# Optimization experiments

Hardware: AMD Instinct MI355X
Metric: run time of the kernel (lower is better)

Reference implementation:

```python
import jax, jax.numpy as jnp
import numpy as np

B, S, D = 2, 4096, 512
H, DK, DV = 8, 64, 64
LN_EPS = 1e-5
ATTN_EPS = 1e-6


def layer_norm(x, g, b):
    mu = jnp.mean(x, axis=-1, keepdims=True)
    var = jnp.var(x, axis=-1, keepdims=True)
    return (x - mu) * jax.lax.rsqrt(var + LN_EPS) * g + b


def setup_inputs() -> dict:
    key = jax.random.key(0)
    ks = jax.random.split(key, 12)
    s = 1.0 / np.sqrt(D)
    inp = {
        "Q": jax.random.normal(ks[0], (B, S, D), jnp.float32),
        "K": jax.random.normal(ks[1], (B, S, D), jnp.float32),
        "V": jax.random.normal(ks[2], (B, S, D), jnp.float32),
        "W_q": jax.random.normal(ks[3], (D, H * DK), jnp.float32) * s,
        "W_k": jax.random.normal(ks[4], (D, H * DK), jnp.float32) * s,
        "W_v": jax.random.normal(ks[5], (D, H * DV), jnp.float32) * s,
        "W_o": jax.random.normal(ks[6], (H * DV, D), jnp.float32) * s,
        "ln1_g": jnp.ones((D,), jnp.float32),
        "ln1_b": jnp.zeros((D,), jnp.float32),
        "ln2_g": jnp.ones((D,), jnp.float32),
        "ln2_b": jnp.zeros((D,), jnp.float32),
        "w1": jax.random.normal(ks[7], (4 * D, D), jnp.float32) * s,  # torch Linear: (out, in)
        "b1": jnp.zeros((4 * D,), jnp.float32),
        "w2": jax.random.normal(ks[8], (D, 4 * D), jnp.float32) * (1.0 / np.sqrt(4 * D)),
        "b2": jnp.zeros((D,), jnp.float32),
    }
    return inp


def reference(Q, K, V, W_q, W_k, W_v, W_o, ln1_g, ln1_b, ln2_g, ln2_b, w1, b1, w2, b2):
    Qn = layer_norm(Q, ln1_g, ln1_b)
    # project and split heads: [B,S,H,dk] -> [B,H,S,dk]
    q = (Qn @ W_q).reshape(B, S, H, DK).transpose(0, 2, 1, 3)
    k = (K @ W_k).reshape(B, S, H, DK).transpose(0, 2, 1, 3)
    v = (V @ W_v).reshape(B, S, H, DV).transpose(0, 2, 1, 3)
    scores = jnp.einsum("bhqd,bhkd->bhqk", q, k) / (np.sqrt(DK) + ATTN_EPS)
    attn = jax.nn.softmax(scores, axis=-1)  # same as max-subtract softmax
    ctx = jnp.einsum("bhqk,bhkd->bhqd", attn, v)
    ctx = ctx.transpose(0, 2, 1, 3).reshape(B, S, H * DV)
    att_out = ctx @ W_o  # dropout = identity (eval)
    X = Q + att_out
    Xn = layer_norm(X, ln2_g, ln2_b)
    h = jax.nn.gelu(Xn @ w1.T + b1, approximate=False)
    ffn = h @ w2.T + b2
    return X + ffn
```

## Files before the change

kernel.cpp:

```cpp
#include <hip/hip_runtime.h>

typedef unsigned short u16;
typedef __attribute__((ext_vector_type(8))) short short8;
typedef __attribute__((ext_vector_type(4))) float f32x4;

struct __align__(8) us4 { u16 x, y, z, w; };
struct __align__(8) ui2 { unsigned x, y; };

#define CEXP (1.44269504089f / (8.0f + 1e-6f))

__device__ __forceinline__ u16 f2bf(float f) {
  unsigned u = __builtin_bit_cast(unsigned, f);
  unsigned r = (u + 0x7FFFu + ((u >> 16) & 1u)) >> 16;
  return (u16)r;
}

__device__ __forceinline__ unsigned pack_bf2_trunc(float a, float b) {
  return __builtin_amdgcn_perm(__builtin_bit_cast(unsigned, b),
                               __builtin_bit_cast(unsigned, a), 0x07060302u);
}

__device__ __forceinline__ void async_load16(const void* g, void* l) {
  __builtin_amdgcn_global_load_lds((const __attribute__((address_space(1))) void*)g,
                                   (__attribute__((address_space(3))) void*)l, 16, 0, 0);
}

__global__ void prep_weights(const float* __restrict__ Wq, const float* __restrict__ Wk,
                             const float* __restrict__ Wv, const float* __restrict__ Wo,
                             const float* __restrict__ w1, const float* __restrict__ w2,
                             u16* __restrict__ wqkvT, u16* __restrict__ woT,
                             u16* __restrict__ w1b, u16* __restrict__ w2b) {
  const int z = blockIdx.y;
  const int stride = gridDim.x * blockDim.x;
  const int i0 = blockIdx.x * blockDim.x + threadIdx.x;
  if (z < 4) {
    const float* src = z == 0 ? Wq : z == 1 ? Wk : z == 2 ? Wv : Wo;
    u16* dst = z < 3 ? wqkvT + z * 512 * 512 : woT;
    const float scale = (z == 0) ? CEXP : 1.0f;
    for (int i = i0; i < 512 * 512; i += stride) {
      int k = i >> 9, n = i & 511;
      dst[(size_t)n * 512 + k] = f2bf(src[i] * scale);
    }
  } else {
    const float* src = z == 4 ? w1 : w2;
    u16* dst = z == 4 ? w1b : w2b;
    for (int i = i0; i < 2048 * 512; i += stride) dst[i] = f2bf(src[i]);
  }
}

template <bool KV>
__launch_bounds__(128)
__global__ void ln_cast(const float* __restrict__ X, const float* __restrict__ gw,
                        const float* __restrict__ bw, u16* __restrict__ Y,
                        const float* __restrict__ Kin, const float* __restrict__ Vin,
                        u16* __restrict__ Kb, u16* __restrict__ Vb) {
  const int row = blockIdx.x, t = threadIdx.x;
  const size_t base = (size_t)row * 512;
  float4 x = ((const float4*)(X + base))[t];
  float s = x.x + x.y + x.z + x.w;
  float ss = x.x * x.x + x.y * x.y + x.z * x.z + x.w * x.w;
#pragma unroll
  for (int off = 32; off > 0; off >>= 1) {
    s += __shfl_xor(s, off);
    ss += __shfl_xor(ss, off);
  }
  __shared__ float red[4];
  if ((t & 63) == 0) { red[(t >> 6) * 2] = s; red[(t >> 6) * 2 + 1] = ss; }
  __syncthreads();
  const float tot = red[0] + red[2], tss = red[1] + red[3];
  const float mu = tot * (1.0f / 512.0f);
  const float var = tss * (1.0f / 512.0f) - mu * mu;
  const float rs = rsqrtf(var + 1e-5f);
  float4 g4 = ((const float4*)gw)[t];
  float4 b4 = ((const float4*)bw)[t];
  us4 o;
  o.x = f2bf((x.x - mu) * rs * g4.x + b4.x);
  o.y = f2bf((x.y - mu) * rs * g4.y + b4.y);
  o.z = f2bf((x.z - mu) * rs * g4.z + b4.z);
  o.w = f2bf((x.w - mu) * rs * g4.w + b4.w);
  ((us4*)(Y + base))[t] = o;
  if constexpr (KV) {
    float4 k4 = ((const float4*)(Kin + base))[t];
    float4 v4 = ((const float4*)(Vin + base))[t];
    us4 ko, vo;
    ko.x = f2bf(k4.x); ko.y = f2bf(k4.y); ko.z = f2bf(k4.z); ko.w = f2bf(k4.w);
    vo.x = f2bf(v4.x); vo.y = f2bf(v4.y); vo.z = f2bf(v4.z); vo.w = f2bf(v4.w);
    ((us4*)(Kb + base))[t] = ko;
    ((us4*)(Vb + base))[t] = vo;
  }
}

__launch_bounds__(256, 3)
__global__ void gemm_qkv(const u16* __restrict__ Aq, const u16* __restrict__ Ak,
                         const u16* __restrict__ Av, const u16* __restrict__ Bt,
                         u16* __restrict__ qb, u16* __restrict__ kb, u16* __restrict__ vtb) {
  __shared__ __align__(16) u16 sA[128 * 32];
  __shared__ __align__(16) u16 sB[128 * 32];
  const int tid = threadIdx.x;
  const int wave = tid >> 6, lane = tid & 63;
  const int l15 = lane & 15, quad = lane >> 4;
  const int qsw = (quad ^ ((l15 >> 1) & 3)) * 8;
  const int m0 = blockIdx.x * 128, n0 = blockIdx.y * 128;
  const int sel = n0 >> 9;
  const u16* A = sel == 0 ? Aq : sel == 1 ? Ak : Av;
  const int wm = (wave >> 1) * 64, wn = (wave & 1) * 64;
  const int u0 = wave * 64 + lane, u1 = u0 + 256;
  const int sw0 = ((u0 & 3) ^ ((u0 >> 3) & 3)) * 8;
  const int K = 512;

  const u16* a0 = A + (size_t)(m0 + (u0 >> 2)) * K + sw0;
  const u16* a1 = A + (size_t)(m0 + (u1 >> 2)) * K + sw0;
  const u16* b0 = Bt + (size_t)(n0 + (u0 >> 2)) * K + sw0;
  const u16* b1p = Bt + (size_t)(n0 + (u1 >> 2)) * K + sw0;

  f32x4 acc[4][4] = {};
  for (int k0 = 0; k0 < K; k0 += 32) {
    async_load16(a0 + k0, &sA[wave * 512]);
    async_load16(a1 + k0, &sA[2048 + wave * 512]);
    async_load16(b0 + k0, &sB[wave * 512]);
    async_load16(b1p + k0, &sB[2048 + wave * 512]);
    __syncthreads();
    short8 af[4], bfr[4];
#pragma unroll
    for (int i = 0; i < 4; i++)
      af[i] = *(const short8*)&sA[(wm + i * 16 + l15) * 32 + qsw];
#pragma unroll
    for (int j = 0; j < 4; j++)
      bfr[j] = *(const short8*)&sB[(wn + j * 16 + l15) * 32 + qsw];
#pragma unroll
    for (int i = 0; i < 4; i++)
#pragma unroll
      for (int j = 0; j < 4; j++)
        acc[i][j] = __builtin_amdgcn_mfma_f32_16x16x32_bf16(af[i], bfr[j], acc[i][j], 0, 0, 0);
    __syncthreads();
  }

#pragma unroll
  for (int i = 0; i < 4; i++) {
#pragma unroll
    for (int j = 0; j < 4; j++) {
      const int ocol = ((n0 + wn) & 511) + j * 16 + l15;
      const int row0 = m0 + wm + i * 16 + quad * 4;
      if (sel < 2) {
        u16* C = sel == 0 ? qb : kb;
#pragma unroll
        for (int r = 0; r < 4; r++) C[(size_t)(row0 + r) * 512 + ocol] = f2bf(acc[i][j][r]);
      } else {
        const int b = row0 >> 12, s0 = row0 & 4095;
        const int hh = ocol >> 6, cc = ocol & 63;
        us4 pk;
        pk.x = f2bf(acc[i][j][0]); pk.y = f2bf(acc[i][j][1]);
        pk.z = f2bf(acc[i][j][2]); pk.w = f2bf(acc[i][j][3]);
        *(us4*)&vtb[((size_t)((b * 8 + hh) * 64 + cc) << 12) + s0] = pk;
      }
    }
  }
}

template <int EP, int TN, int LB>
__launch_bounds__(256, LB)
__global__ void gemm_bt(const u16* __restrict__ A, const u16* __restrict__ Bt,
                        int M, int N, int K, void* __restrict__ Cp,
                        const float* __restrict__ bias, const float* __restrict__ res) {
  constexpr int MI = (TN == 128) ? 4 : 2;
  __shared__ __align__(16) u16 sA[128 * 32];
  __shared__ __align__(16) u16 sB[TN * 32];
  const int tid = threadIdx.x;
  const int wave = tid >> 6, lane = tid & 63;
  const int l15 = lane & 15, quad = lane >> 4;
  const int qsw = (quad ^ ((l15 >> 1) & 3)) * 8;
  const int m0 = blockIdx.x * 128, n0 = blockIdx.y * TN;
  const int wm = (TN == 128) ? (wave >> 1) * 64 : wave * 32;
  const int wn = (TN == 128) ? (wave & 1) * 64 : 0;
  const int u0 = wave * 64 + lane, u1 = u0 + 256;
  const int sw0 = ((u0 & 3) ^ ((u0 >> 3) & 3)) * 8;

  const u16* a0 = A + (size_t)(m0 + (u0 >> 2)) * K + sw0;
  const u16* a1 = A + (size_t)(m0 + (u1 >> 2)) * K + sw0;
  const u16* b0 = Bt + (size_t)(n0 + (u0 >> 2)) * K + sw0;

  f32x4 acc[MI][4] = {};
  for (int k0 = 0; k0 < K; k0 += 32) {
    async_load16(a0 + k0, &sA[wave * 512]);
    async_load16(a1 + k0, &sA[2048 + wave * 512]);
    async_load16(b0 + k0, &sB[wave * 512]);
    if constexpr (TN == 128) {
      const u16* b1p = Bt + (size_t)(n0 + (u1 >> 2)) * K + sw0;
      async_load16(b1p + k0, &sB[2048 + wave * 512]);
    }
    __syncthreads();
    short8 af[MI], bfr[4];
#pragma unroll
    for (int i = 0; i < MI; i++)
      af[i] = *(const short8*)&sA[(wm + i * 16 + l15) * 32 + qsw];
#pragma unroll
    for (int j = 0; j < 4; j++)
      bfr[j] = *(const short8*)&sB[(wn + j * 16 + l15) * 32 + qsw];
#pragma unroll
    for (int i = 0; i < MI; i++)
#pragma unroll
      for (int j = 0; j < 4; j++)
        acc[i][j] = __builtin_amdgcn_mfma_f32_16x16x32_bf16(af[i], bfr[j], acc[i][j], 0, 0, 0);
    __syncthreads();
  }

#pragma unroll
  for (int i = 0; i < MI; i++) {
#pragma unroll
    for (int j = 0; j < 4; j++) {
      const int col = n0 + wn + j * 16 + l15;
      const int row0 = m0 + wm + i * 16 + quad * 4;
      if (EP == 2) {
        float* C = (float*)Cp;
#pragma unroll
        for (int r = 0; r < 4; r++) {
          size_t idx = (size_t)(row0 + r) * N + col;
          C[idx] = acc[i][j][r] + res[idx];
        }
      } else if (EP == 3) {
        u16* C = (u16*)Cp;
        const float bv = bias[col];
#pragma unroll
        for (int r = 0; r < 4; r++) {
          float xx = acc[i][j][r] + bv;
          float gl = 0.5f * xx * (1.0f + erff(xx * 0.70710678118f));
          C[(size_t)(row0 + r) * N + col] = f2bf(gl);
        }
      } else {
        float* C = (float*)Cp;
        const float bv = bias[col];
#pragma unroll
        for (int r = 0; r < 4; r++) {
          size_t idx = (size_t)(row0 + r) * N + col;
          C[idx] = acc[i][j][r] + bv + res[idx];
        }
      }
    }
  }
}

__launch_bounds__(256, 3)
__global__ void attn_kernel(const u16* __restrict__ qb, const u16* __restrict__ kb,
                            const u16* __restrict__ vtb, float* __restrict__ po,
                            float* __restrict__ pl) {
  __shared__ __align__(16) u16 sK[2 * 128 * 32];
  __shared__ __align__(16) u16 sV[4 * 64 * 32];
  __shared__ __align__(16) u16 sP[4 * 32 * 40];
  const int tid = threadIdx.x;
  const int wave = tid >> 6, lane = tid & 63;
  const int l15 = lane & 15, quad = lane >> 4;
  const int qsw = (quad ^ ((l15 >> 1) & 3)) * 8;
  const int bh = blockIdx.y, b = bh >> 3, h = bh & 7;
  const int q0 = blockIdx.x * 128;
  const int ks = blockIdx.z;
  const size_t rb = (size_t)b * 4096;

  short8 qf[2][2];
#pragma unroll
  for (int mi = 0; mi < 2; mi++)
#pragma unroll
    for (int kk = 0; kk < 2; kk++) {
      int row = q0 + wave * 32 + mi * 16 + l15;
      qf[mi][kk] = *(const short8*)&qb[(rb + row) * 512 + h * 64 + kk * 32 + quad * 8];
    }

  f32x4 o_t[2][4] = {};
  float l_part[2] = {0.f, 0.f};
  u16* myP = &sP[wave * 32 * 40];

  for (int jt = 0; jt < 16; jt++) {
    const int j0 = ks * 2048 + jt * 128;
#pragma unroll
    for (int r = 0; r < 4; r++) {
      int u = r * 256 + wave * 64 + lane;
      int kk = u >> 9, key = (u >> 2) & 127, c8 = (u & 3) ^ ((u >> 3) & 3);
      async_load16(&kb[(rb + j0 + key) * 512 + h * 64 + kk * 32 + c8 * 8],
                   &sK[(r * 256 + wave * 64) * 8]);
    }
#pragma unroll
    for (int r = 0; r < 4; r++) {
      int u = r * 256 + wave * 64 + lane;
      int kk = u >> 8, vc = (u >> 2) & 63, c8 = (u & 3) ^ ((u >> 3) & 3);
      async_load16(&vtb[((size_t)(bh * 64 + vc)) * 4096 + j0 + kk * 32 + c8 * 8],
                   &sV[(r * 256 + wave * 64) * 8]);
    }
    __syncthreads();

#pragma unroll
    for (int kk = 0; kk < 4; kk++) {
#pragma unroll
      for (int nh = 0; nh < 2; nh++) {
        const int ni = kk * 2 + nh;
        short8 af0 = *(const short8*)&sK[(ni * 16 + l15) * 32 + qsw];
        short8 af1 = *(const short8*)&sK[4096 + (ni * 16 + l15) * 32 + qsw];
#pragma unroll
        for (int mi = 0; mi < 2; mi++) {
          f32x4 st = {};
          st = __builtin_amdgcn_mfma_f32_16x16x32_bf16(af0, qf[mi][0], st, 0, 0, 0);
          st = __builtin_amdgcn_mfma_f32_16x16x32_bf16(af1, qf[mi][1], st, 0, 0, 0);
          float p0 = __builtin_amdgcn_exp2f(st[0]);
          float p1 = __builtin_amdgcn_exp2f(st[1]);
          float p2 = __builtin_amdgcn_exp2f(st[2]);
          float p3 = __builtin_amdgcn_exp2f(st[3]);
          l_part[mi] += (p0 + p1) + (p2 + p3);
          ui2 wv;
          wv.x = pack_bf2_trunc(p0, p1);
          wv.y = pack_bf2_trunc(p2, p3);
          *(ui2*)&myP[(mi * 16 + l15) * 40 + nh * 16 + quad * 4] = wv;
        }
      }
      asm volatile("s_waitcnt lgkmcnt(0)" ::: "memory");
      short8 pf[2], vf[4];
#pragma unroll
      for (int mi = 0; mi < 2; mi++)
        pf[mi] = *(const short8*)&myP[(mi * 16 + l15) * 40 + quad * 8];
#pragma unroll
      for (int vi = 0; vi < 4; vi++)
        vf[vi] = *(const short8*)&sV[kk * 2048 + (vi * 16 + l15) * 32 + qsw];
#pragma unroll
      for (int mi = 0; mi < 2; mi++)
#pragma unroll
        for (int vi = 0; vi < 4; vi++)
          o_t[mi][vi] = __builtin_amdgcn_mfma_f32_16x16x32_bf16(vf[vi], pf[mi], o_t[mi][vi], 0, 0, 0);
    }
    __syncthreads();
  }

#pragma unroll
  for (int mi = 0; mi < 2; mi++) {
    float l = l_part[mi];
    l += __shfl_xor(l, 16);
    l += __shfl_xor(l, 32);
    const int qrow = q0 + wave * 32 + mi * 16 + l15;
    if (quad == 0) pl[(size_t)ks * 65536 + (rb + qrow) * 8 + h] = l;
#pragma unroll
    for (int vi = 0; vi < 4; vi++)
      *(f32x4*)&po[(size_t)ks * 4194304 + (rb + qrow) * 512 + h * 64 + vi * 16 + quad * 4] =
          o_t[mi][vi];
  }
}

__launch_bounds__(128)
__global__ void attn_merge(const float* __restrict__ po, const float* __restrict__ pl,
                           u16* __restrict__ ctx) {
  const int row = blockIdx.x, t = threadIdx.x;
  const int col = t * 4, h = col >> 6;
  const size_t idx = (size_t)row * 512 + col;
  const float l = pl[row * 8 + h] + pl[65536 + row * 8 + h];
  f32x4 a = *(const f32x4*)&po[idx];
  f32x4 c = *(const f32x4*)&po[4194304 + idx];
  const float inv = 1.0f / l;
  us4 o;
  o.x = f2bf((a[0] + c[0]) * inv);
  o.y = f2bf((a[1] + c[1]) * inv);
  o.z = f2bf((a[2] + c[2]) * inv);
  o.w = f2bf((a[3] + c[3]) * inv);
  *(us4*)&ctx[idx] = o;
}

extern "C" void kernel_launch(void* const* d_in, const int* in_sizes, int n_in,
                              void* d_out, int out_size, void* d_ws, size_t ws_size,
                              hipStream_t stream) {
  (void)in_sizes; (void)n_in; (void)out_size; (void)ws_size;
  const float* Q = (const float*)d_in[0];
  const float* K = (const float*)d_in[1];
  const float* V = (const float*)d_in[2];
  const float* W_q = (const float*)d_in[3];
  const float* W_k = (const float*)d_in[4];
  const float* W_v = (const float*)d_in[5];
  const float* W_o = (const float*)d_in[6];
  const float* ln1_g = (const float*)d_in[7];
  const float* ln1_b = (const float*)d_in[8];
  const float* ln2_g = (const float*)d_in[9];
  const float* ln2_b = (const float*)d_in[10];
  const float* w1 = (const float*)d_in[11];
  const float* b1 = (const float*)d_in[12];
  const float* w2 = (const float*)d_in[13];
  const float* b2 = (const float*)d_in[14];

  char* w = (char*)d_ws;
  const size_t MB = 1u << 20;
  u16* wqkvT = (u16*)(w);
  u16* woT = (u16*)(w + 3 * MB / 2);
  u16* w1b = (u16*)(w + 2 * MB);
  u16* w2b = (u16*)(w + 4 * MB);
  u16* Qn  = (u16*)(w + 6 * MB);
  u16* Kb  = (u16*)(w + 14 * MB);
  u16* Vb  = (u16*)(w + 22 * MB);
  u16* qb  = (u16*)(w + 30 * MB);
  u16* kb  = (u16*)(w + 38 * MB);
  u16* vtb = (u16*)(w + 46 * MB);
  u16* ctx = (u16*)(w + 54 * MB);
  float* X = (float*)(w + 94 * MB);
  float* po = (float*)(w + 62 * MB);
  float* pl = (float*)(w + 6 * MB);
  u16* Xn  = (u16*)(w + 6 * MB + MB);
  Xn = (u16*)(w + 6 * MB);
  u16* hb  = (u16*)(w + 14 * MB);

  prep_weights<<<dim3(128, 6), 256, 0, stream>>>(W_q, W_k, W_v, W_o, w1, w2,
                                                 wqkvT, woT, w1b, w2b);
  ln_cast<true><<<8192, 128, 0, stream>>>(Q, ln1_g, ln1_b, Qn, K, V, Kb, Vb);
  gemm_qkv<<<dim3(64, 12), 256, 0, stream>>>(Qn, Kb, Vb, wqkvT, qb, kb, vtb);
  attn_kernel<<<dim3(32, 16, 2), 256, 0, stream>>>(qb, kb, vtb, po, pl);
  attn_merge<<<8192, 128, 0, stream>>>(po, pl, ctx);
  gemm_bt<2, 64, 3><<<dim3(64, 8), 256, 0, stream>>>(ctx, woT, 8192, 512, 512, X, nullptr, Q);
  ln_cast<false><<<8192, 128, 0, stream>>>(X, ln2_g, ln2_b, Xn, nullptr, nullptr, nullptr, nullptr);
  gemm_bt<3, 128, 3><<<dim3(64, 16), 256, 0, stream>>>(Xn, w1b, 8192, 2048, 512, hb, b1, nullptr);
  gemm_bt<4, 64, 3><<<dim3(64, 8), 256, 0, stream>>>(hb, w2b, 8192, 512, 2048, (float*)d_out, b2, X);
}
```

Baseline: 351.4 us.

## Tile weight transpose through LDS, vectorize casts, widen output-projection GEMM tiles

The weight-prep kernel now transposes the 512x512 projection weights via a padded 64x64 shared-memory tile, giving coalesced float4 reads and 8-byte writes instead of strided scalar stores. The FFN weight cast is vectorized to float4 loads and us4 stores. The Wo and w2 GEMMs switch to 128-wide N tiles with a different third template parameter, which halves their grid to 256 blocks. This may cut CU occupancy and change the register footprint per block.

```diff
diff --git a/kernel.cpp b/kernel.cpp
--- a/kernel.cpp
+++ b/kernel.cpp
@@ -31,20 +31,42 @@
                              u16* __restrict__ wqkvT, u16* __restrict__ woT,
                              u16* __restrict__ w1b, u16* __restrict__ w2b) {
   const int z = blockIdx.y;
-  const int stride = gridDim.x * blockDim.x;
-  const int i0 = blockIdx.x * blockDim.x + threadIdx.x;
+  const int t = threadIdx.x;
   if (z < 4) {
     const float* src = z == 0 ? Wq : z == 1 ? Wk : z == 2 ? Wv : Wo;
     u16* dst = z < 3 ? wqkvT + z * 512 * 512 : woT;
     const float scale = (z == 0) ? CEXP : 1.0f;
-    for (int i = i0; i < 512 * 512; i += stride) {
-      int k = i >> 9, n = i & 511;
-      dst[(size_t)n * 512 + k] = f2bf(src[i] * scale);
+    __shared__ float tl[64][65];
+    const int ti = blockIdx.x >> 3, tj = blockIdx.x & 7;
+    const int tx = t & 15, ty = t >> 4;
+#pragma unroll
+    for (int rr = 0; rr < 4; rr++) {
+      const int row = rr * 16 + ty;
+      float4 v = *(const float4*)&src[(size_t)(ti * 64 + row) * 512 + tj * 64 + tx * 4];
+      tl[row][tx * 4 + 0] = v.x; tl[row][tx * 4 + 1] = v.y;
+      tl[row][tx * 4 + 2] = v.z; tl[row][tx * 4 + 3] = v.w;
+    }
+    __syncthreads();
+#pragma unroll
+    for (int rr = 0; rr < 4; rr++) {
+      const int row = rr * 16 + ty;
+      us4 o;
+      o.x = f2bf(tl[tx * 4 + 0][row] * scale);
+      o.y = f2bf(tl[tx * 4 + 1][row] * scale);
+      o.z = f2bf(tl[tx * 4 + 2][row] * scale);
+      o.w = f2bf(tl[tx * 4 + 3][row] * scale);
+      *(us4*)&dst[(size_t)(tj * 64 + row) * 512 + ti * 64 + tx * 4] = o;
     }
   } else {
     const float* src = z == 4 ? w1 : w2;
     u16* dst = z == 4 ? w1b : w2b;
-    for (int i = i0; i < 2048 * 512; i += stride) dst[i] = f2bf(src[i]);
+    const int stride = gridDim.x * blockDim.x;
+    for (int i = blockIdx.x * blockDim.x + t; i < 2048 * 512 / 4; i += stride) {
+      float4 v = ((const float4*)src)[i];
+      us4 o;
+      o.x = f2bf(v.x); o.y = f2bf(v.y); o.z = f2bf(v.z); o.w = f2bf(v.w);
+      ((us4*)dst)[i] = o;
+    }
   }
 }
 
@@ -391,21 +413,20 @@
   u16* kb  = (u16*)(w + 38 * MB);
   u16* vtb = (u16*)(w + 46 * MB);
   u16* ctx = (u16*)(w + 54 * MB);
-  float* X = (float*)(w + 94 * MB);
   float* po = (float*)(w + 62 * MB);
   float* pl = (float*)(w + 6 * MB);
-  u16* Xn  = (u16*)(w + 6 * MB + MB);
-  Xn = (u16*)(w + 6 * MB);
+  float* X = (float*)(w + 94 * MB);
+  u16* Xn  = (u16*)(w + 6 * MB);
   u16* hb  = (u16*)(w + 14 * MB);
 
-  prep_weights<<<dim3(128, 6), 256, 0, stream>>>(W_q, W_k, W_v, W_o, w1, w2,
-                                                 wqkvT, woT, w1b, w2b);
+  prep_weights<<<dim3(64, 6), 256, 0, stream>>>(W_q, W_k, W_v, W_o, w1, w2,
+                                                wqkvT, woT, w1b, w2b);
   ln_cast<true><<<8192, 128, 0, stream>>>(Q, ln1_g, ln1_b, Qn, K, V, Kb, Vb);
   gemm_qkv<<<dim3(64, 12), 256, 0, stream>>>(Qn, Kb, Vb, wqkvT, qb, kb, vtb);
   attn_kernel<<<dim3(32, 16, 2), 256, 0, stream>>>(qb, kb, vtb, po, pl);
   attn_merge<<<8192, 128, 0, stream>>>(po, pl, ctx);
-  gemm_bt<2, 64, 3><<<dim3(64, 8), 256, 0, stream>>>(ctx, woT, 8192, 512, 512, X, nullptr, Q);
+  gemm_bt<2, 128, 2><<<dim3(64, 4), 256, 0, stream>>>(ctx, woT, 8192, 512, 512, X, nullptr, Q);
   ln_cast<false><<<8192, 128, 0, stream>>>(X, ln2_g, ln2_b, Xn, nullptr, nullptr, nullptr, nullptr);
   gemm_bt<3, 128, 3><<<dim3(64, 16), 256, 0, stream>>>(Xn, w1b, 8192, 2048, 512, hb, b1, nullptr);
-  gemm_bt<4, 64, 3><<<dim3(64, 8), 256, 0, stream>>>(hb, w2b, 8192, 512, 2048, (float*)d_out, b2, X);
-}
+  gemm_bt<4, 128, 2><<<dim3(64, 4), 256, 0, stream>>>(hb, w2b, 8192, 512, 2048, (float*)d_out, b2, X);
+}
```

New measurement: 344.5 us. 2.0% less time.
